# Performance work log

Hardware: AMD Instinct MI355X
Metric: run time of the kernel (lower is better)

## Reference

```python
import jax, jax.numpy as jnp
import numpy as np

NN = 1024  # nodes per LSTM layer (equal across layers, required by gating broadcast)


def setup_inputs() -> dict:
    key = jax.random.key(0)
    ks = jax.random.split(key, 8)
    T, B, V, E = 64, 64, 32000, 512
    ip = 0.3
    inputs = jax.random.normal(ks[0], (T, B, V), dtype=jnp.float32) * 0.1
    embedding_matrix = jax.random.normal(ks[1], (V, E), dtype=jnp.float32) * (ip * np.sqrt(1.0 / V))
    lstm_w0 = jax.random.normal(ks[2], (E + NN, 4 * NN), dtype=jnp.float32) * (ip * np.sqrt(1.0 / (E + NN)))
    lstm_b0 = jnp.zeros((4 * NN,), dtype=jnp.float32)
    lstm_w1 = jax.random.normal(ks[3], (2 * NN, 4 * NN), dtype=jnp.float32) * (ip * np.sqrt(1.0 / (2 * NN)))
    lstm_b1 = jnp.zeros((4 * NN,), dtype=jnp.float32)
    gates_w = jax.random.normal(ks[4], (2 * NN, 2), dtype=jnp.float32) * (ip * np.sqrt(1.0 / (2 * NN)))
    out_w = jax.random.normal(ks[5], (NN, V), dtype=jnp.float32) * (ip * np.sqrt(1.0 / NN))
    out_b = jnp.zeros((V,), dtype=jnp.float32)
    return dict(inputs=inputs, embedding_matrix=embedding_matrix,
                lstm_w0=lstm_w0, lstm_b0=lstm_b0, lstm_w1=lstm_w1, lstm_b1=lstm_b1,
                gates_w=gates_w, out_w=out_w, out_b=out_b)


def _cell(x, h, c, W, b):
    # concat -> matmul -> bias -> split [3*NN sigmoid | NN tanh] -> gate update
    z = jnp.concatenate([x, h], axis=1) @ W + b
    sig = jax.nn.sigmoid(z[:, : 3 * NN])
    g = jnp.tanh(z[:, 3 * NN:])
    f, i, o = sig[:, :NN], sig[:, NN:2 * NN], sig[:, 2 * NN:]
    c_new = f * c + i * g
    h_new = o * jnp.tanh(c_new)
    return h_new, c_new


def _forward(inputs, embedding_matrix, lstm_w0, lstm_b0, lstm_w1, lstm_b1, gates_w, out_w, out_b):
    T, B, V = inputs.shape
    emb = jnp.einsum('tbv,ve->tbe', inputs, embedding_matrix)  # [T,B,E]

    def step(carry, e_t):
        h0, c0, h1, c1 = carry
        h0, c0 = _cell(e_t, h0, c0, lstm_w0, lstm_b0)
        h1, c1 = _cell(h0, h1, c1, lstm_w1, lstm_b1)
        return (h0, c0, h1, c1), (h0, h1)

    zeros = jnp.zeros((B, NN), dtype=inputs.dtype)
    _, (h0s, h1s) = jax.lax.scan(step, (zeros, zeros, zeros, zeros), emb)
    h0_flat = h0s.reshape(T * B, NN)  # concat along time == stacked reshape
    h1_flat = h1s.reshape(T * B, NN)
    full = jnp.concatenate([h0_flat, h1_flat], axis=1)  # [T*B, 2*NN]
    gates = jax.nn.sigmoid(full @ gates_w)               # [T*B, 2]
    gated = gates[:, 0:1] * h0_flat + gates[:, 1:2] * h1_flat
    logits = gated @ out_w + out_b                       # [T*B, V]
    return logits


def reference(inputs, embedding_matrix, lstm_w0, lstm_b0, lstm_w1, lstm_b1, gates_w, out_w, out_b):
    return _forward(inputs, embedding_matrix, lstm_w0, lstm_b0, lstm_w1, lstm_b1, gates_w, out_w, out_b)
```

## Files before the change

### kernel.cpp

```cpp
#include <hip/hip_runtime.h>
#include <math.h>

typedef __attribute__((ext_vector_type(8))) short bf16x8;
typedef __attribute__((ext_vector_type(4))) float f32x4;
typedef __attribute__((ext_vector_type(8))) _Float16 f16x8;
typedef unsigned short ushort_t;

#define T_STEPS 64
#define BATCH   64
#define VOCAB   32000
#define EMB     512
#define HID     1024
#define G4      4096

__device__ __forceinline__ unsigned short f2bf(float x) {
    unsigned u = __builtin_bit_cast(unsigned, x);
    u += 0x7FFFu + ((u >> 16) & 1u);
    return (unsigned short)(u >> 16);
}
__device__ __forceinline__ float bf2f(unsigned short h) {
    unsigned u = ((unsigned)h) << 16;
    return __builtin_bit_cast(float, u);
}
__device__ __forceinline__ unsigned pack2(unsigned short a, unsigned short b) {
    return (unsigned)a | ((unsigned)b << 16);
}
__device__ __forceinline__ unsigned short f2h(float x) {
    return __builtin_bit_cast(unsigned short, (_Float16)x);
}
__device__ __forceinline__ float h2f(unsigned short h) {
    return (float)__builtin_bit_cast(_Float16, h);
}
__device__ __forceinline__ f32x4 ntload4(const float* p) {
    return __builtin_nontemporal_load((const f32x4*)p);
}

__device__ __forceinline__ size_t packA_off(int row, int k, int M16) {
    return ((size_t)((k >> 5) * M16 + (row >> 4))) * 512 +
           ((k & 31) >> 3) * 128 + (row & 15) * 8 + (k & 7);
}

__launch_bounds__(512, 2)
__global__ void gemm_emb(const float* __restrict__ A, const ushort_t* __restrict__ Bp,
                         float* __restrict__ C) {
    __shared__ _Float16 AhS[2][128][40];
    const int tid = threadIdx.x;
    const int row0 = blockIdx.x * 128;
    const int z = blockIdx.y;
    const int kBeg = z * 4000;
    const int kb8  = z * 500;
    C += (size_t)z * 4096 * EMB;

    const int l = tid & 63, w = tid >> 6;
    const int wm = w >> 2, wn = w & 3;
    const int lr = l & 15, lk = l >> 4;

    const int ar = tid >> 2, ak8 = (tid & 3) << 3;
    const float* Abase = A + (size_t)(row0 + ar) * VOCAB + kBeg + ak8;

    f32x4 acc[4][8];
#pragma unroll
    for (int m = 0; m < 4; ++m)
#pragma unroll
        for (int n = 0; n < 8; ++n)
#pragma unroll
            for (int r = 0; r < 4; ++r) acc[m][n][r] = 0.f;

    auto loadB = [&](int k, f16x8* dst) {
#pragma unroll
        for (int n = 0; n < 8; ++n) {
            int g = wn * 8 + n;
            dst[n] = *(const f16x8*)(Bp + ((size_t)g * 4000 + kb8 + k * 4 + lk) * 128 + lr * 8);
        }
    };
    auto loadA = [&](int k, f32x4& v0, f32x4& v1) {
        const float* ap = Abase + k * 32;
        v0 = ntload4(ap); v1 = ntload4(ap + 4);
    };
    auto storeA = [&](int buf, f32x4 v0, f32x4 v1) {
        f16x8 hv;
        hv[0] = (_Float16)v0[0]; hv[1] = (_Float16)v0[1];
        hv[2] = (_Float16)v0[2]; hv[3] = (_Float16)v0[3];
        hv[4] = (_Float16)v1[0]; hv[5] = (_Float16)v1[1];
        hv[6] = (_Float16)v1[2]; hv[7] = (_Float16)v1[3];
        *(f16x8*)&AhS[buf][ar][ak8] = hv;
    };
    auto mfmaStep = [&](int buf, f16x8* bset) {
        f16x8 a[4];
#pragma unroll
        for (int m = 0; m < 4; ++m)
            a[m] = *(const f16x8*)&AhS[buf][wm * 64 + m * 16 + lr][lk * 8];
#pragma unroll
        for (int m = 0; m < 4; ++m)
#pragma unroll
            for (int n = 0; n < 8; ++n)
                acc[m][n] = __builtin_amdgcn_mfma_f32_16x16x32_f16(a[m], bset[n], acc[m][n], 0, 0, 0);
    };

    f16x8 bA[8], bB[8];
    f32x4 a0A, a1A, a0B, a1B;
    {
        f32x4 t0, t1;
        loadA(0, t0, t1); storeA(0, t0, t1);
        loadA(1, a0A, a1A);
        loadB(0, bA); loadB(1, bB);
        __syncthreads();
    }
    for (int k = 0; k < 124; k += 2) {
        if (k + 2 < 125) loadA(k + 2, a0B, a1B);
        mfmaStep(0, bA);
        if (k + 2 < 125) loadB(k + 2, bA);
        storeA(1, a0A, a1A);
        __syncthreads();
        if (k + 3 < 125) loadA(k + 3, a0A, a1A);
        mfmaStep(1, bB);
        if (k + 3 < 125) loadB(k + 3, bB);
        if (k + 2 < 125) storeA(0, a0B, a1B);
        __syncthreads();
    }
    mfmaStep(0, bA);

    constexpr float invScale = 1.f / 256.f;
#pragma unroll
    for (int n = 0; n < 8; ++n) {
        int col = (wn * 8 + n) * 16 + lr;
#pragma unroll
        for (int m = 0; m < 4; ++m) {
            int rbase = row0 + wm * 64 + m * 16 + lk * 4;
#pragma unroll
            for (int r = 0; r < 4; ++r)
                C[(size_t)(rbase + r) * EMB + col] = acc[m][n][r] * invScale;
        }
    }
}

template<int BM, int BN, int NW_M, int NW_N, bool NTA, bool NTC>
__launch_bounds__(NW_M * NW_N * 64)
__global__ void gemm_a32b16(const float* __restrict__ A, const ushort_t* __restrict__ Bp,
                            float* __restrict__ C, int lda, int ldc, int K8,
                            int KCHUNK, size_t chunkStride, float invScale) {
    constexpr int THREADS = NW_M * NW_N * 64;
    constexpr int MF = BM / NW_M / 16;
    constexpr int NF = BN / NW_N / 16;
    __shared__ _Float16 AhS[BM][40];

    const int tid  = threadIdx.x;
    const int row0 = blockIdx.y * BM;
    const int gBase = blockIdx.x * (BN / 16);
    const int kBeg = blockIdx.z * KCHUNK;
    C += (size_t)blockIdx.z * chunkStride;

    const int l = tid & 63, w = tid >> 6;
    const int wm = w / NW_N, wn = w % NW_N;
    const int lr = l & 15, lk = l >> 4;

    f32x4 acc[MF][NF];
#pragma unroll
    for (int m = 0; m < MF; ++m)
#pragma unroll
        for (int n = 0; n < NF; ++n)
#pragma unroll
            for (int r = 0; r < 4; ++r) acc[m][n][r] = 0.f;

    constexpr int AI = BM * 4 / THREADS;

    for (int k0 = 0; k0 < KCHUNK; k0 += 32) {
#pragma unroll
        for (int i = 0; i < AI; ++i) {
            int f = tid + i * THREADS;
            int r = f >> 2, k8 = (f & 3) << 3;
            const float* ap = A + (size_t)(row0 + r) * lda + kBeg + k0 + k8;
            f32x4 v0, v1;
            if (NTA) { v0 = ntload4(ap); v1 = ntload4(ap + 4); }
            else     { v0 = *(const f32x4*)ap; v1 = *(const f32x4*)(ap + 4); }
            f16x8 hv;
            hv[0] = (_Float16)v0[0]; hv[1] = (_Float16)v0[1];
            hv[2] = (_Float16)v0[2]; hv[3] = (_Float16)v0[3];
            hv[4] = (_Float16)v1[0]; hv[5] = (_Float16)v1[1];
            hv[6] = (_Float16)v1[2]; hv[7] = (_Float16)v1[3];
            *(f16x8*)&AhS[r][k8] = hv;
        }
        __syncthreads();
        const size_t kRow = (size_t)((kBeg + k0) >> 3) + lk;
        f16x8 a[MF], b[NF];
#pragma unroll
        for (int n = 0; n < NF; ++n) {
            int g = gBase + wn * NF + n;
            b[n] = *(const f16x8*)(Bp + ((size_t)g * K8 + kRow) * 128 + lr * 8);
        }
#pragma unroll
        for (int m = 0; m < MF; ++m)
            a[m] = *(const f16x8*)&AhS[wm * MF * 16 + m * 16 + lr][lk * 8];
#pragma unroll
        for (int m = 0; m < MF; ++m)
#pragma unroll
            for (int n = 0; n < NF; ++n)
                acc[m][n] = __builtin_amdgcn_mfma_f32_16x16x32_f16(a[m], b[n], acc[m][n], 0, 0, 0);
        __syncthreads();
    }

#pragma unroll
    for (int n = 0; n < NF; ++n) {
        int col = (gBase + wn * NF + n) * 16 + lr;
#pragma unroll
        for (int m = 0; m < MF; ++m) {
            int rbase = row0 + wm * MF * 16 + m * 16 + lk * 4;
#pragma unroll
            for (int r = 0; r < 4; ++r) {
                float v = acc[m][n][r] * invScale;
                float* cp = &C[(size_t)(rbase + r) * ldc + col];
                if (NTC) __builtin_nontemporal_store(v, cp);
                else *cp = v;
            }
        }
    }
}

__global__ void reduce8(const float* __restrict__ zp, float* __restrict__ out, size_t cs) {
    size_t i = ((size_t)blockIdx.x * 256 + threadIdx.x) * 4;
    f32x4 a = *(const f32x4*)(zp + i);
#pragma unroll
    for (int c = 1; c < 8; ++c) {
        f32x4 b = *(const f32x4*)(zp + c * cs + i);
        a += b;
    }
    *(f32x4*)(out + i) = a;
}

template<bool PERM>
__launch_bounds__(256)
__global__ void wcv16(const float* __restrict__ W, ushort_t* __restrict__ Wp,
                      int Krows, int ldW, float scale) {
    __shared__ float tile[32][33];
    const int k0 = blockIdx.x * 32;
    const int n0 = blockIdx.y * 32;
    const int tid = threadIdx.x;
#pragma unroll
    for (int i = 0; i < 4; ++i) {
        int idx = tid + i * 256;
        int r = idx >> 5, c = idx & 31;
        tile[r][c] = W[(size_t)(k0 + r) * ldW + n0 + c];
    }
    __syncthreads();
    const int rn = tid >> 3;
    const int cq = (tid & 7) * 4;
    unsigned short h[4];
#pragma unroll
    for (int j = 0; j < 4; ++j) h[j] = f2h(tile[cq + j][rn] * scale);
    const int n = n0 + rn;
    const int p = PERM ? (((n & 1023) >> 2) * 16 + (n >> 10) * 4 + (n & 3)) : n;
    const int k = k0 + cq;
    size_t off = ((size_t)(p >> 4) * (Krows >> 3) + (k >> 3)) * 128 + (p & 15) * 8 + (k & 7);
    uint2 hp; hp.x = pack2(h[0], h[1]); hp.y = pack2(h[2], h[3]);
    *(uint2*)(Wp + off) = hp;
}

template<int K>
__device__ __forceinline__ void lstm_body(
        float* red, int cg,
        const ushort_t* Ah, const ushort_t* Al,
        const ushort_t* Wp,
        const float* xpart, const float* bias,
        float* c_state, float* histF,
        ushort_t* d1h, ushort_t* d1l,
        ushort_t* d2h, ushort_t* d2l) {
    const int tid = threadIdx.x;
    const int l = tid & 63, w = tid >> 6;
    const int lr = l & 15, lk = l >> 4;
    constexpr int spw = K >> 8;
    const size_t wbase = (size_t)cg * (K >> 3) * 128 + lk * 128 + lr * 8;

    f32x4 acc[4];
#pragma unroll
    for (int m = 0; m < 4; ++m)
#pragma unroll
        for (int r = 0; r < 4; ++r) acc[m][r] = 0.f;

    const int s0 = w * spw;
    const ushort_t* wptr = Wp + wbase + (size_t)s0 * 512;
    const ushort_t* aptr = Ah + (size_t)s0 * 4 * 512 + l * 8;
    const ushort_t* lptr = Al + (size_t)s0 * 4 * 512 + l * 8;
#pragma unroll
    for (int s = 0; s < spw; ++s) {
        f16x8 bw = *(const f16x8*)(wptr + (size_t)s * 512);
#pragma unroll
        for (int m = 0; m < 4; ++m) {
            f16x8 ah = *(const f16x8*)(aptr + (size_t)(s * 4 + m) * 512);
            f16x8 al = *(const f16x8*)(lptr + (size_t)(s * 4 + m) * 512);
            acc[m] = __builtin_amdgcn_mfma_f32_16x16x32_f16(ah, bw, acc[m], 0, 0, 0);
            acc[m] = __builtin_amdgcn_mfma_f32_16x16x32_f16(al, bw, acc[m], 0, 0, 0);
        }
    }
#pragma unroll
    for (int m = 0; m < 4; ++m)
        *(f32x4*)&red[(w * 64 + l) * 20 + m * 4] = acc[m];
    __syncthreads();

    if (tid < 256) {
        const int r = tid >> 2, v = tid & 3;
        const int m = r >> 4, lkq = (r >> 2) & 3, reg = r & 3;
        const int u = cg * 4 + v;
        constexpr float invS = 1.f / 65536.f;
        float z[4];
#pragma unroll
        for (int j = 0; j < 4; ++j) {
            const int c = j * 4 + v;
            float s = 0.f;
#pragma unroll
            for (int ww = 0; ww < 8; ++ww)
                s += red[(ww * 64 + lkq * 16 + c) * 20 + m * 4 + reg];
            s = s * invS + bias[j * 1024 + u];
            if (xpart)
                s += __builtin_nontemporal_load(&xpart[(size_t)r * 4096 + j * 1024 + u]);
            z[j] = s;
        }
        float f = 1.f / (1.f + expf(-z[0]));
        float i = 1.f / (1.f + expf(-z[1]));
        float o = 1.f / (1.f + expf(-z[2]));
        float g = tanhf(z[3]);
        const int cidx = r * 1024 + u;
        float cn = f * c_state[cidx] + i * g;
        c_state[cidx] = cn;
        float hn = o * tanhf(cn);
        __builtin_nontemporal_store(hn, &histF[cidx]);
        float hs = hn * 256.f;
        unsigned short hh = f2h(hs);
        unsigned short hl = f2h(hs - h2f(hh));
        size_t o1 = packA_off(r, u, 4);
        d1h[o1] = hh; d1l[o1] = hl;
        if (d2h) {
            size_t o2 = packA_off(r, u, 4);
            d2h[o2] = hh; d2l[o2] = hl;
        }
    }
    __syncthreads();
}

__launch_bounds__(512)
__global__ void lstm_pair(int active0, int active1,
        const ushort_t* Ah0, const ushort_t* Al0, const ushort_t* Wp0,
        const float* xpart0, const float* bias0,
        float* c0, float* hist0,
        ushort_t* d1h0, ushort_t* d1l0, ushort_t* d2h0, ushort_t* d2l0,
        const ushort_t* Ah1, const ushort_t* Al1, const ushort_t* Wp1,
        const float* bias1, float* c1, float* hist1,
        ushort_t* d1h1, ushort_t* d1l1) {
    __shared__ float red[512 * 20];
    const int b = blockIdx.x;
    if (b < 256) {
        if (!active0) return;
        lstm_body<1024>(red, b, Ah0, Al0, Wp0, xpart0, bias0,
                        c0, hist0, d1h0, d1l0, d2h0, d2l0);
    } else {
        if (!active1) return;
        lstm_body<2048>(red, b - 256, Ah1, Al1, Wp1, nullptr, bias1,
                        c1, hist1, d1h1, d1l1, nullptr, nullptr);
    }
}

__launch_bounds__(256)
__global__ void gates_gated(const float* __restrict__ h0s, const float* __restrict__ h1s,
                            const float* __restrict__ gw,
                            ushort_t* __restrict__ gA16) {
    const int r = blockIdx.x;
    const int tid = threadIdx.x;
    const float* h0r = h0s + (size_t)r * HID;
    const float* h1r = h1s + (size_t)r * HID;
    float p0 = 0.f, p1 = 0.f;
    for (int k = tid; k < HID; k += 256) {
        float v0 = h0r[k], v1 = h1r[k];
        p0 += v0 * gw[2 * k]     + v1 * gw[2 * (HID + k)];
        p1 += v0 * gw[2 * k + 1] + v1 * gw[2 * (HID + k) + 1];
    }
#pragma unroll
    for (int off = 32; off; off >>= 1) {
        p0 += __shfl_down(p0, off);
        p1 += __shfl_down(p1, off);
    }
    __shared__ float s0[4], s1[4];
    __shared__ float gg[2];
    if ((tid & 63) == 0) { s0[tid >> 6] = p0; s1[tid >> 6] = p1; }
    __syncthreads();
    if (tid == 0) {
        float a = s0[0] + s0[1] + s0[2] + s0[3];
        float b = s1[0] + s1[1] + s1[2] + s1[3];
        gg[0] = 1.f / (1.f + expf(-a));
        gg[1] = 1.f / (1.f + expf(-b));
    }
    __syncthreads();
    float g0 = gg[0], g1 = gg[1];
    const int n0 = tid * 4;
    unsigned short h[4];
#pragma unroll
    for (int j = 0; j < 4; ++j) {
        int n = n0 + j;
        h[j] = f2h((g0 * h0r[n] + g1 * h1r[n]) * 256.f);
    }
    uint2 hp; hp.x = pack2(h[0], h[1]); hp.y = pack2(h[2], h[3]);
    *(uint2*)(gA16 + packA_off(r, n0, 256)) = hp;
}

__launch_bounds__(512)
__global__ void gemm_out_v4(const ushort_t* __restrict__ gA16, const ushort_t* __restrict__ Bp,
                            const float* __restrict__ bias, float* __restrict__ C) {
    __shared__ ushort_t AL[2][8192];
    __shared__ ushort_t BL[2][4096];

    const int tid = threadIdx.x;
    const int lin = (blockIdx.x & 7) * 500 + (blockIdx.x >> 3);
    const int bi = lin / 250, bj = lin % 250;
    const int row0 = bi * 256, col0 = bj * 128;

    const int l = tid & 63, w = tid >> 6;
    const int wm = w >> 1, wn = w & 1;
    const int lr = l & 15, lk = l >> 4;

    const int aOff = tid * 8;
    const size_t bBase = (size_t)(bj * 8 + (tid >> 6)) * 16384 + (tid & 63) * 8;

    f32x4 acc[4][4];
#pragma unroll
    for (int m = 0; m < 4; ++m)
#pragma unroll
        for (int n = 0; n < 4; ++n)
#pragma unroll
            for (int r = 0; r < 4; ++r) acc[m][n][r] = 0.f;

    {
        const size_t cA = ((size_t)(bi * 16)) * 512;
        uint4 a0 = *(const uint4*)(gA16 + cA + aOff);
        uint4 a1 = *(const uint4*)(gA16 + cA + 4096 + aOff);
        uint4 b0 = *(const uint4*)(Bp + bBase);
        *(uint4*)&AL[0][aOff] = a0;
        *(uint4*)&AL[0][4096 + aOff] = a1;
        *(uint4*)&BL[0][aOff & 4095] = b0;
    }
    __syncthreads();

    uint4 rA0, rA1, rB;
    for (int k32 = 0; k32 < 32; ++k32) {
        const int cur = k32 & 1, nxt = cur ^ 1;
        const bool hasNext = (k32 < 31);
        if (hasNext) {
            const size_t cA = ((size_t)((k32 + 1) * 256 + bi * 16)) * 512;
            rA0 = *(const uint4*)(gA16 + cA + aOff);
            rA1 = *(const uint4*)(gA16 + cA + 4096 + aOff);
            rB  = *(const uint4*)(Bp + bBase + (size_t)(k32 + 1) * 512);
        }
        f16x8 a[4], b[4];
#pragma unroll
        for (int m = 0; m < 4; ++m)
            a[m] = *(const f16x8*)&AL[cur][(wm * 4 + m) * 512 + l * 8];
#pragma unroll
        for (int n = 0; n < 4; ++n)
            b[n] = *(const f16x8*)&BL[cur][(wn * 4 + n) * 512 + l * 8];
#pragma unroll
        for (int m = 0; m < 4; ++m)
#pragma unroll
            for (int n = 0; n < 4; ++n)
                acc[m][n] = __builtin_amdgcn_mfma_f32_16x16x32_f16(a[m], b[n], acc[m][n], 0, 0, 0);
        if (hasNext) {
            *(uint4*)&AL[nxt][aOff] = rA0;
            *(uint4*)&AL[nxt][4096 + aOff] = rA1;
            *(uint4*)&BL[nxt][aOff & 4095] = rB;
        }
        __syncthreads();
    }

    constexpr float invScale = 1.f / 65536.f;
#pragma unroll
    for (int n = 0; n < 4; ++n) {
        int col = col0 + wn * 64 + n * 16 + lr;
        float bv = bias[col];
#pragma unroll
        for (int m = 0; m < 4; ++m) {
            int rbase = row0 + wm * 64 + m * 16 + lk * 4;
#pragma unroll
            for (int r = 0; r < 4; ++r)
                __builtin_nontemporal_store(acc[m][n][r] * invScale + bv,
                                            &C[(size_t)(rbase + r) * VOCAB + col]);
        }
    }
}

extern "C" void kernel_launch(void* const* d_in, const int* in_sizes, int n_in,
                              void* d_out, int out_size, void* d_ws, size_t ws_size,
                              hipStream_t stream) {
    const float* inputs = (const float*)d_in[0];
    const float* embm   = (const float*)d_in[1];
    const float* w0     = (const float*)d_in[2];
    const float* b0     = (const float*)d_in[3];
    const float* w1     = (const float*)d_in[4];
    const float* b1     = (const float*)d_in[5];
    const float* gw     = (const float*)d_in[6];
    const float* outw   = (const float*)d_in[7];
    const float* outb   = (const float*)d_in[8];
    float* logits = (float*)d_out;

    float* ws    = (float*)d_ws;
    float* emb   = ws;
    float* h0s   = ws + 2097152;
    float* h1s   = ws + 6291456;
    ushort_t* gA16 = (ushort_t*)(ws + 10485760);
    float* c0    = ws + 14942208;
    float* c1    = ws + 15007744;
    ushort_t* hpB = (ushort_t*)(ws + 15073280);
    ushort_t* outw16 = (ushort_t*)(ws + 15466496);

    ushort_t* hp0h[2] = { hpB,            hpB + 65536 };
    ushort_t* hp0l[2] = { hpB + 131072,   hpB + 196608 };
    ushort_t* hp1h[2] = { hpB + 262144,   hpB + 393216 };
    ushort_t* hp1l[2] = { hpB + 524288,   hpB + 655360 };

    float* zpEmb = (float*)d_out;
    float* z0x   = (float*)d_out + 16777216;
    ushort_t* wt0 = (ushort_t*)((float*)d_out + 33554432);
    ushort_t* wt1 = wt0 + 4194304;
    ushort_t* embm16 = wt1 + 8388608;
    ushort_t* w0x16  = embm16 + 16384000;

    (void)hipMemsetAsync(c0, 0, (size_t)524288 * sizeof(float), stream);

    wcv16<false><<<dim3(1000, 16), 256, 0, stream>>>(embm, embm16, VOCAB, EMB, 256.f);
    wcv16<false><<<dim3(16, 128), 256, 0, stream>>>(w0, w0x16, EMB, G4, 256.f);
    wcv16<false><<<dim3(32, 1000), 256, 0, stream>>>(outw, outw16, HID, VOCAB, 256.f);
    wcv16<true><<<dim3(32, 128), 256, 0, stream>>>(w0 + (size_t)512 * G4, wt0, 1024, G4, 256.f);
    wcv16<true><<<dim3(64, 128), 256, 0, stream>>>(w1, wt1, 2048, G4, 256.f);

    gemm_emb<<<dim3(32, 8), 512, 0, stream>>>(inputs, embm16, zpEmb);
    reduce8<<<2048, 256, 0, stream>>>(zpEmb, emb, (size_t)4096 * EMB);

    gemm_a32b16<128, 128, 2, 2, false, true><<<dim3(32, 32, 1), 256, 0, stream>>>(
        emb, w0x16, z0x, EMB, G4, EMB / 8, EMB, 0, 1.f / 256.f);

    for (int t = 0; t <= T_STEPS; ++t) {
        const int p0 = t & 1, q0 = (t + 1) & 1;
        const int s  = t - 1, ss = s < 0 ? 0 : s;
        const int p1 = ss & 1, q1 = (ss + 1) & 1;
        lstm_pair<<<512, 512, 0, stream>>>(
            (t < T_STEPS) ? 1 : 0, (t >= 1) ? 1 : 0,
            hp0h[p0], hp0l[p0], wt0,
            z0x + (size_t)(t < T_STEPS ? t : 0) * 262144, b0,
            c0, h0s + (size_t)(t < T_STEPS ? t : 0) * 65536,
            hp0h[q0], hp0l[q0], hp1h[p0], hp1l[p0],
            hp1h[p1], hp1l[p1], wt1,
            b1, c1, h1s + (size_t)ss * 65536,
            hp1h[q1] + 65536, hp1l[q1] + 65536);
    }

    gates_gated<<<4096, 256, 0, stream>>>(h0s, h1s, gw, gA16);

    gemm_out_v4<<<4000, 512, 0, stream>>>(gA16, outw16, outb, logits);
}
```

Baseline: 1.728 ms.

## Process two column groups per LSTM block to reuse activation fragments

Each LSTM step block now computes two adjacent 4-unit column groups instead of one. The loaded A (hi/lo) fragments are reused across two weight fragments, and the grid drops from 512 to 256 blocks. All 512 threads now take part in the gate epilogue instead of half of them. This halves redundant activation loads but cuts block-level parallelism on a 256-CU device, and it enlarges shared memory and register use.

```diff
diff --git a/kernel.cpp b/kernel.cpp
--- a/kernel.cpp
+++ b/kernel.cpp
@@ -256,8 +256,8 @@
 }
 
 template<int K>
-__device__ __forceinline__ void lstm_body(
-        float* red, int cg,
+__device__ __forceinline__ void lstm_body2(
+        float* red, int cg0,
         const ushort_t* Ah, const ushort_t* Al,
         const ushort_t* Wp,
         const float* xpart, const float* bias,
@@ -268,38 +268,48 @@
     const int l = tid & 63, w = tid >> 6;
     const int lr = l & 15, lk = l >> 4;
     constexpr int spw = K >> 8;
-    const size_t wbase = (size_t)cg * (K >> 3) * 128 + lk * 128 + lr * 8;
-
-    f32x4 acc[4];
+    const size_t lane_off = (size_t)lk * 128 + lr * 8;
+    const size_t wb0 = (size_t)cg0 * (K >> 3) * 128 + lane_off;
+    const size_t wb1 = (size_t)(cg0 + 1) * (K >> 3) * 128 + lane_off;
+
+    f32x4 acc0[4], acc1[4];
 #pragma unroll
     for (int m = 0; m < 4; ++m)
 #pragma unroll
-        for (int r = 0; r < 4; ++r) acc[m][r] = 0.f;
+        for (int r = 0; r < 4; ++r) { acc0[m][r] = 0.f; acc1[m][r] = 0.f; }
 
     const int s0 = w * spw;
-    const ushort_t* wptr = Wp + wbase + (size_t)s0 * 512;
+    const ushort_t* wptr0 = Wp + wb0 + (size_t)s0 * 512;
+    const ushort_t* wptr1 = Wp + wb1 + (size_t)s0 * 512;
     const ushort_t* aptr = Ah + (size_t)s0 * 4 * 512 + l * 8;
     const ushort_t* lptr = Al + (size_t)s0 * 4 * 512 + l * 8;
 #pragma unroll
     for (int s = 0; s < spw; ++s) {
-        f16x8 bw = *(const f16x8*)(wptr + (size_t)s * 512);
+        f16x8 bw0 = *(const f16x8*)(wptr0 + (size_t)s * 512);
+        f16x8 bw1 = *(const f16x8*)(wptr1 + (size_t)s * 512);
 #pragma unroll
         for (int m = 0; m < 4; ++m) {
             f16x8 ah = *(const f16x8*)(aptr + (size_t)(s * 4 + m) * 512);
             f16x8 al = *(const f16x8*)(lptr + (size_t)(s * 4 + m) * 512);
-            acc[m] = __builtin_amdgcn_mfma_f32_16x16x32_f16(ah, bw, acc[m], 0, 0, 0);
-            acc[m] = __builtin_amdgcn_mfma_f32_16x16x32_f16(al, bw, acc[m], 0, 0, 0);
-        }
-    }
-#pragma unroll
-    for (int m = 0; m < 4; ++m)
-        *(f32x4*)&red[(w * 64 + l) * 20 + m * 4] = acc[m];
+            acc0[m] = __builtin_amdgcn_mfma_f32_16x16x32_f16(ah, bw0, acc0[m], 0, 0, 0);
+            acc0[m] = __builtin_amdgcn_mfma_f32_16x16x32_f16(al, bw0, acc0[m], 0, 0, 0);
+            acc1[m] = __builtin_amdgcn_mfma_f32_16x16x32_f16(ah, bw1, acc1[m], 0, 0, 0);
+            acc1[m] = __builtin_amdgcn_mfma_f32_16x16x32_f16(al, bw1, acc1[m], 0, 0, 0);
+        }
+    }
+#pragma unroll
+    for (int m = 0; m < 4; ++m) {
+        *(f32x4*)&red[(w * 64 + l) * 36 + m * 4]      = acc0[m];
+        *(f32x4*)&red[(w * 64 + l) * 36 + 16 + m * 4] = acc1[m];
+    }
     __syncthreads();
 
-    if (tid < 256) {
-        const int r = tid >> 2, v = tid & 3;
+    {
+        const int gl = tid >> 8;
+        const int tt = tid & 255;
+        const int r = tt >> 2, v = tt & 3;
         const int m = r >> 4, lkq = (r >> 2) & 3, reg = r & 3;
-        const int u = cg * 4 + v;
+        const int u = (cg0 + gl) * 4 + v;
         constexpr float invS = 1.f / 65536.f;
         float z[4];
 #pragma unroll
@@ -308,7 +318,7 @@
             float s = 0.f;
 #pragma unroll
             for (int ww = 0; ww < 8; ++ww)
-                s += red[(ww * 64 + lkq * 16 + c) * 20 + m * 4 + reg];
+                s += red[(ww * 64 + lkq * 16 + c) * 36 + gl * 16 + m * 4 + reg];
             s = s * invS + bias[j * 1024 + u];
             if (xpart)
                 s += __builtin_nontemporal_load(&xpart[(size_t)r * 4096 + j * 1024 + u]);
@@ -345,16 +355,16 @@
         const ushort_t* Ah1, const ushort_t* Al1, const ushort_t* Wp1,
         const float* bias1, float* c1, float* hist1,
         ushort_t* d1h1, ushort_t* d1l1) {
-    __shared__ float red[512 * 20];
+    __shared__ float red[512 * 36];
     const int b = blockIdx.x;
-    if (b < 256) {
+    if (b < 128) {
         if (!active0) return;
-        lstm_body<1024>(red, b, Ah0, Al0, Wp0, xpart0, bias0,
-                        c0, hist0, d1h0, d1l0, d2h0, d2l0);
+        lstm_body2<1024>(red, b * 2, Ah0, Al0, Wp0, xpart0, bias0,
+                         c0, hist0, d1h0, d1l0, d2h0, d2l0);
     } else {
         if (!active1) return;
-        lstm_body<2048>(red, b - 256, Ah1, Al1, Wp1, nullptr, bias1,
-                        c1, hist1, d1h1, d1l1, nullptr, nullptr);
+        lstm_body2<2048>(red, (b - 128) * 2, Ah1, Al1, Wp1, nullptr, bias1,
+                         c1, hist1, d1h1, d1l1, nullptr, nullptr);
     }
 }
 
@@ -537,7 +547,7 @@
         const int p0 = t & 1, q0 = (t + 1) & 1;
         const int s  = t - 1, ss = s < 0 ? 0 : s;
         const int p1 = ss & 1, q1 = (ss + 1) & 1;
-        lstm_pair<<<512, 512, 0, stream>>>(
+        lstm_pair<<<256, 512, 0, stream>>>(
             (t < T_STEPS) ? 1 : 0, (t >= 1) ? 1 : 0,
             hp0h[p0], hp0l[p0], wt0,
             z0x + (size_t)(t < T_STEPS ? t : 0) * 262144, b0,
```

Measured after the change: 1.487 ms, median of 2. 1.16x faster.

## Process multiple column groups per block in LSTM step kernel to reuse activations

Applied to the files above, without the earlier changes.

Each LSTM block now computes NG column groups (4 for layer 0, 2 for layer 1) instead of one. Each A-fragment load from the hidden-state buffers then feeds NG MFMAs, which cuts redundant activation traffic. The grid shrinks from 512 to 192 blocks per step, with a larger shared reduction buffer. The trade-off is fewer blocks to fill the 256 CUs, more registers per thread, and more LDS per block, which may lower occupancy on a latency-bound recurrent step.

```diff
diff --git a/kernel.cpp b/kernel.cpp
--- a/kernel.cpp
+++ b/kernel.cpp
@@ -255,9 +255,9 @@
     *(uint2*)(Wp + off) = hp;
 }
 
-template<int K>
-__device__ __forceinline__ void lstm_body(
-        float* red, int cg,
+template<int K, int NG>
+__device__ __forceinline__ void lstm_bodyN(
+        float* red, int cg0,
         const ushort_t* Ah, const ushort_t* Al,
         const ushort_t* Wp,
         const float* xpart, const float* bias,
@@ -268,38 +268,57 @@
     const int l = tid & 63, w = tid >> 6;
     const int lr = l & 15, lk = l >> 4;
     constexpr int spw = K >> 8;
-    const size_t wbase = (size_t)cg * (K >> 3) * 128 + lk * 128 + lr * 8;
-
-    f32x4 acc[4];
-#pragma unroll
-    for (int m = 0; m < 4; ++m)
-#pragma unroll
-        for (int r = 0; r < 4; ++r) acc[m][r] = 0.f;
+    constexpr int RS = NG * 16 + 4;
+    const size_t lane_off = (size_t)lk * 128 + lr * 8;
+
+    const ushort_t* wptr[NG];
+#pragma unroll
+    for (int g = 0; g < NG; ++g)
+        wptr[g] = Wp + (size_t)(cg0 + g) * (K >> 3) * 128 + lane_off + (size_t)(w * spw) * 512;
+
+    f32x4 acc[NG][4];
+#pragma unroll
+    for (int g = 0; g < NG; ++g)
+#pragma unroll
+        for (int m = 0; m < 4; ++m)
+#pragma unroll
+            for (int r = 0; r < 4; ++r) acc[g][m][r] = 0.f;
 
     const int s0 = w * spw;
-    const ushort_t* wptr = Wp + wbase + (size_t)s0 * 512;
     const ushort_t* aptr = Ah + (size_t)s0 * 4 * 512 + l * 8;
     const ushort_t* lptr = Al + (size_t)s0 * 4 * 512 + l * 8;
 #pragma unroll
     for (int s = 0; s < spw; ++s) {
-        f16x8 bw = *(const f16x8*)(wptr + (size_t)s * 512);
+        f16x8 bw[NG];
+#pragma unroll
+        for (int g = 0; g < NG; ++g)
+            bw[g] = *(const f16x8*)(wptr[g] + (size_t)s * 512);
 #pragma unroll
         for (int m = 0; m < 4; ++m) {
             f16x8 ah = *(const f16x8*)(aptr + (size_t)(s * 4 + m) * 512);
             f16x8 al = *(const f16x8*)(lptr + (size_t)(s * 4 + m) * 512);
-            acc[m] = __builtin_amdgcn_mfma_f32_16x16x32_f16(ah, bw, acc[m], 0, 0, 0);
-            acc[m] = __builtin_amdgcn_mfma_f32_16x16x32_f16(al, bw, acc[m], 0, 0, 0);
-        }
-    }
-#pragma unroll
-    for (int m = 0; m < 4; ++m)
-        *(f32x4*)&red[(w * 64 + l) * 20 + m * 4] = acc[m];
+#pragma unroll
+            for (int g = 0; g < NG; ++g) {
+                acc[g][m] = __builtin_amdgcn_mfma_f32_16x16x32_f16(ah, bw[g], acc[g][m], 0, 0, 0);
+                acc[g][m] = __builtin_amdgcn_mfma_f32_16x16x32_f16(al, bw[g], acc[g][m], 0, 0, 0);
+            }
+        }
+    }
+#pragma unroll
+    for (int g = 0; g < NG; ++g)
+#pragma unroll
+        for (int m = 0; m < 4; ++m)
+            *(f32x4*)&red[(w * 64 + l) * RS + g * 16 + m * 4] = acc[g][m];
     __syncthreads();
 
-    if (tid < 256) {
-        const int r = tid >> 2, v = tid & 3;
+#pragma unroll
+    for (int e = 0; e < NG / 2; ++e) {
+        const int uu = tid + e * 512;
+        const int gl = uu >> 8;
+        const int tt = uu & 255;
+        const int r = tt >> 2, v = tt & 3;
         const int m = r >> 4, lkq = (r >> 2) & 3, reg = r & 3;
-        const int u = cg * 4 + v;
+        const int u = (cg0 + gl) * 4 + v;
         constexpr float invS = 1.f / 65536.f;
         float z[4];
 #pragma unroll
@@ -308,7 +327,7 @@
             float s = 0.f;
 #pragma unroll
             for (int ww = 0; ww < 8; ++ww)
-                s += red[(ww * 64 + lkq * 16 + c) * 20 + m * 4 + reg];
+                s += red[(ww * 64 + lkq * 16 + c) * RS + gl * 16 + m * 4 + reg];
             s = s * invS + bias[j * 1024 + u];
             if (xpart)
                 s += __builtin_nontemporal_load(&xpart[(size_t)r * 4096 + j * 1024 + u]);
@@ -345,16 +364,16 @@
         const ushort_t* Ah1, const ushort_t* Al1, const ushort_t* Wp1,
         const float* bias1, float* c1, float* hist1,
         ushort_t* d1h1, ushort_t* d1l1) {
-    __shared__ float red[512 * 20];
+    __shared__ float red[512 * 68];
     const int b = blockIdx.x;
-    if (b < 256) {
+    if (b < 64) {
         if (!active0) return;
-        lstm_body<1024>(red, b, Ah0, Al0, Wp0, xpart0, bias0,
-                        c0, hist0, d1h0, d1l0, d2h0, d2l0);
+        lstm_bodyN<1024, 4>(red, b * 4, Ah0, Al0, Wp0, xpart0, bias0,
+                            c0, hist0, d1h0, d1l0, d2h0, d2l0);
     } else {
         if (!active1) return;
-        lstm_body<2048>(red, b - 256, Ah1, Al1, Wp1, nullptr, bias1,
-                        c1, hist1, d1h1, d1l1, nullptr, nullptr);
+        lstm_bodyN<2048, 2>(red, (b - 64) * 2, Ah1, Al1, Wp1, nullptr, bias1,
+                            c1, hist1, d1h1, d1l1, nullptr, nullptr);
     }
 }
 
@@ -537,7 +556,7 @@
         const int p0 = t & 1, q0 = (t + 1) & 1;
         const int s  = t - 1, ss = s < 0 ? 0 : s;
         const int p1 = ss & 1, q1 = (ss + 1) & 1;
-        lstm_pair<<<512, 512, 0, stream>>>(
+        lstm_pair<<<192, 512, 0, stream>>>(
             (t < T_STEPS) ? 1 : 0, (t >= 1) ? 1 : 0,
             hp0h[p0], hp0l[p0], wt0,
             z0x + (size_t)(t < T_STEPS ? t : 0) * 262144, b0,
```

Measured after the change: 1.637 ms. 5.3% less time.
